# Optimization experiments

Measured on AMD Instinct MI355X. Metric: run time of the kernel, lower is better.

The kernel has to match this reference:

```python
import jax, jax.numpy as jnp
import numpy as np
import math

D_MODEL = 1024
N_HEADS = 16
DK = D_MODEL // N_HEADS


def setup_inputs() -> dict:
    key = jax.random.key(0)
    kx, kqkv, kproj = jax.random.split(key, 3)
    B, T = 4, 2048
    x = jax.random.normal(kx, (B, T, D_MODEL), dtype=jnp.float32)
    # torch Linear weight is [out, in]; y = x @ W.T
    W_qkv = jax.random.normal(kqkv, (3 * D_MODEL, D_MODEL), dtype=jnp.float32) * (1.0 / math.sqrt(D_MODEL))
    W_proj = jax.random.normal(kproj, (D_MODEL, D_MODEL), dtype=jnp.float32) * (1.0 / math.sqrt(D_MODEL))
    return {"x": x, "W_qkv": W_qkv, "W_proj": W_proj}


def reference(x, W_qkv, W_proj):
    B, T, D = x.shape
    qkv = jnp.einsum("btd,ed->bte", x, W_qkv)  # [B,T,3D]
    q, k, v = jnp.split(qkv, 3, axis=-1)
    # [B,T,D] -> [B,H,T,dk]
    def heads(t):
        return t.reshape(B, T, N_HEADS, DK).transpose(0, 2, 1, 3)
    q, k, v = heads(q), heads(k), heads(v)
    scale = 1.0 / math.sqrt(DK)
    att = jnp.einsum("bhqd,bhkd->bhqk", q, k) * scale  # [B,H,T,T]
    att = jax.nn.softmax(att, axis=-1)
    out = jnp.einsum("bhqk,bhkd->bhqd", att, v)  # [B,H,T,dk]
    out = out.transpose(0, 2, 1, 3).reshape(B, T, D)
    return jnp.einsum("btd,ed->bte", out, W_proj)
```

## Files before the change

kernel.cpp:

```cpp
#include <hip/hip_runtime.h>
#include <hip/hip_bf16.h>

#define D_MODEL 1024
#define N_HEADS 16
#define DK 64
#define B_SZ 4
#define T_SEQ 2048
#define M_ROWS (B_SZ * T_SEQ)
#define QK_SCALE_LOG2 0.18033688f

typedef short bf16x8 __attribute__((ext_vector_type(8)));
typedef float f32x4  __attribute__((ext_vector_type(4)));

__device__ inline unsigned short f32_to_bf16(float f) {
    union { float f; unsigned int u; } v; v.f = f;
    unsigned int r = v.u + 0x7fff + ((v.u >> 16) & 1);
    return (unsigned short)(r >> 16);
}
__device__ inline unsigned int pack_bf16x2(float a, float b) {
    __hip_bfloat162 t = __float22bfloat162_rn(make_float2(a, b));
    union { __hip_bfloat162 v; unsigned int u; } c; c.v = t;
    return c.u;
}

__global__ __launch_bounds__(256) void cast_bf16(
    const float* __restrict__ src, unsigned short* __restrict__ dst,
    int n, int nscaled, float s)
{
    for (int i = (blockIdx.x * 256 + threadIdx.x) * 4; i < n;
         i += gridDim.x * 256 * 4) {
        float4 v = *(const float4*)(src + i);
        const float sc = (i < nscaled) ? s : 1.0f;
        ushort4 h;
        h.x = f32_to_bf16(v.x * sc); h.y = f32_to_bf16(v.y * sc);
        h.z = f32_to_bf16(v.z * sc); h.w = f32_to_bf16(v.w * sc);
        *(ushort4*)(dst + i) = h;
    }
}

template <typename OutT>
__global__ __launch_bounds__(256) void gemm_bf16_nt(
    const unsigned short* __restrict__ A, const unsigned short* __restrict__ B,
    OutT* __restrict__ C, int M, int N, int K)
{
    __shared__ __align__(16) unsigned short sA[128 * 32];
    __shared__ __align__(16) unsigned short sB[128 * 32];

    const int t    = threadIdx.x;
    const int wave = t >> 6;
    const int lane = t & 63;
    const int l15  = lane & 15;
    const int quad = lane >> 4;
    const int m0   = blockIdx.y * 128;
    const int n0   = blockIdx.x * 128;

    const unsigned short* gplane = (wave < 2) ? A : B;
    unsigned short* lplane = (wave < 2) ? sA : sB;
    const int row0 = ((wave < 2) ? m0 : n0) + (wave & 1) * 64;
    const int lds0 = (wave & 1) * 2048;
    const unsigned short* gbase =
        gplane + (size_t)(row0 + (lane >> 2)) * K + (lane & 3) * 8;

    f32x4 acc[4][4];
#pragma unroll
    for (int i = 0; i < 4; ++i)
#pragma unroll
        for (int j = 0; j < 4; ++j) acc[i][j] = (f32x4){0.f, 0.f, 0.f, 0.f};

    const int wr = (wave >> 1) * 64;
    const int wc = (wave & 1) * 64;

    for (int k0 = 0; k0 < K; k0 += 32) {
#pragma unroll
        for (int i = 0; i < 4; ++i) {
            __builtin_amdgcn_global_load_lds(
                (const __attribute__((address_space(1))) unsigned int*)
                    (gbase + k0 + (size_t)i * 16 * K),
                (__attribute__((address_space(3))) unsigned int*)
                    (lplane + lds0 + i * 512),
                16, 0, 0);
        }
        __syncthreads();

        bf16x8 a[4], b[4];
#pragma unroll
        for (int f = 0; f < 4; ++f) {
            a[f] = *(const bf16x8*)&sA[(wr + f * 16 + l15) * 32 + quad * 8];
            b[f] = *(const bf16x8*)&sB[(wc + f * 16 + l15) * 32 + quad * 8];
        }
#pragma unroll
        for (int mi = 0; mi < 4; ++mi)
#pragma unroll
            for (int ni = 0; ni < 4; ++ni)
                acc[mi][ni] = __builtin_amdgcn_mfma_f32_16x16x32_bf16(
                    a[mi], b[ni], acc[mi][ni], 0, 0, 0);
        __syncthreads();
    }

#pragma unroll
    for (int mi = 0; mi < 4; ++mi)
#pragma unroll
        for (int r = 0; r < 4; ++r) {
            OutT* crow =
                C + (size_t)(m0 + wr + mi * 16 + quad * 4 + r) * N + n0 + wc + l15;
#pragma unroll
            for (int ni = 0; ni < 4; ++ni) {
                if constexpr (sizeof(OutT) == 2)
                    crow[ni * 16] = (OutT)f32_to_bf16(acc[mi][ni][r]);
                else
                    crow[ni * 16] = (OutT)acc[mi][ni][r];
            }
        }
}

__global__ __launch_bounds__(256) void prep_vt(
    const unsigned short* __restrict__ qkvb, unsigned short* __restrict__ vt)
{
    __shared__ unsigned short VT_s[64][132];
    const int t  = threadIdx.x;
    const int b  = blockIdx.z, h = blockIdx.y;
    const int t0 = blockIdx.x * 128;
    const unsigned short* vb = qkvb + (size_t)(b * T_SEQ) * (3 * D_MODEL)
                               + 2 * D_MODEL + h * DK;
#pragma unroll
    for (int it = 0; it < 8; ++it) {
        const int trow = (t >> 4) + it * 16;
        const int dk0  = (t & 15) * 4;
        ushort4 v = *(const ushort4*)(vb + (size_t)(t0 + trow) * (3 * D_MODEL) + dk0);
        VT_s[dk0 + 0][trow] = v.x; VT_s[dk0 + 1][trow] = v.y;
        VT_s[dk0 + 2][trow] = v.z; VT_s[dk0 + 3][trow] = v.w;
    }
    __syncthreads();

    const int c     = t >> 4;
    const int p8    = c * 8;
    const int sbase = (p8 & ~31) + ((p8 >> 3) & 3) * 4;
    unsigned short* dst =
        vt + (((size_t)((b * N_HEADS + h) * (T_SEQ / 128) + blockIdx.x) * 16 + c)
              * 64) * 8;
#pragma unroll
    for (int dd = 0; dd < 4; ++dd) {
        const int d = (t & 15) + dd * 16;
        ushort4 a  = *(const ushort4*)&VT_s[d][sbase];
        ushort4 b4 = *(const ushort4*)&VT_s[d][sbase + 16];
        union { ushort4 p[2]; uint4 v; } pk;
        pk.p[0] = a; pk.p[1] = b4;
        *(uint4*)(dst + d * 8) = pk.v;
    }
}

__global__ __launch_bounds__(256, 4) void attn_mfma(
    const unsigned short* __restrict__ qkvb,
    const unsigned short* __restrict__ vt,
    unsigned short* __restrict__ ob)
{
    __shared__ __align__(16) unsigned short Ksw[2][128 * 64];

    const int t    = threadIdx.x;
    const int wave = t >> 6;
    const int lane = t & 63;
    const int l15  = t & 15;
    const int quad = lane >> 4;
    const int swz  = l15 & 7;

    const int b  = blockIdx.z;
    const int h  = blockIdx.y;
    const int q0 = blockIdx.x * 128;

    bf16x8 qa[2][2];
#pragma unroll
    for (int qs = 0; qs < 2; ++qs) {
        const unsigned short* qrow =
            qkvb + ((size_t)(b * T_SEQ) + q0 + wave * 32 + qs * 16 + l15)
                   * (3 * D_MODEL) + h * DK;
        qa[qs][0] = *(const bf16x8*)(qrow + quad * 8);
        qa[qs][1] = *(const bf16x8*)(qrow + 32 + quad * 8);
    }

    f32x4 O[2][4], Lacc[2];
#pragma unroll
    for (int qs = 0; qs < 2; ++qs) {
        Lacc[qs] = (f32x4){0.f, 0.f, 0.f, 0.f};
#pragma unroll
        for (int nd = 0; nd < 4; ++nd) O[qs][nd] = (f32x4){0.f, 0.f, 0.f, 0.f};
    }

    const short one_bf = (short)0x3F80;
    const bf16x8 ones8 = {one_bf, one_bf, one_bf, one_bf,
                          one_bf, one_bf, one_bf, one_bf};

    const unsigned short* kbase =
        qkvb + (size_t)(b * T_SEQ) * (3 * D_MODEL) + D_MODEL + h * DK;
    const unsigned short* vbase =
        vt + (size_t)(b * N_HEADS + h) * DK * T_SEQ;

    const int krl  = wave * 32 + (lane >> 3);
    const int kcol = ((lane & 7) ^ (lane >> 3)) * 8;

#pragma unroll
    for (int i = 0; i < 4; ++i) {
        const int rk = krl + i * 8;
        __builtin_amdgcn_global_load_lds(
            (const __attribute__((address_space(1))) unsigned int*)
                (kbase + (size_t)rk * (3 * D_MODEL) + kcol),
            (__attribute__((address_space(3))) unsigned int*)
                (&Ksw[0][(wave * 4 + i) * 512]),
            16, 0, 0);
    }

    const int NT = T_SEQ / 128;
    for (int tile = 0; tile < NT; ++tile) {
        __syncthreads();

        if (tile + 1 < NT) {
            const int c0n = (tile + 1) * 128;
            const int nb  = (tile + 1) & 1;
#pragma unroll
            for (int i = 0; i < 4; ++i) {
                const int rk = krl + i * 8;
                __builtin_amdgcn_global_load_lds(
                    (const __attribute__((address_space(1))) unsigned int*)
                        (kbase + (size_t)(c0n + rk) * (3 * D_MODEL) + kcol),
                    (__attribute__((address_space(3))) unsigned int*)
                        (&Ksw[nb][(wave * 4 + i) * 512]),
                    16, 0, 0);
            }
        }

        const int cb = tile & 1;
        const unsigned short* vtile = vbase + (size_t)tile * (16 * 64 * 8);
        const unsigned short* vlane = vtile + quad * 512 + l15 * 8;
#pragma unroll
        for (int half = 0; half < 2; ++half) {
            f32x4 S[2][4];
#pragma unroll
            for (int qs = 0; qs < 2; ++qs)
#pragma unroll
                for (int nf = 0; nf < 4; ++nf) S[qs][nf] = (f32x4){0.f, 0.f, 0.f, 0.f};

            __builtin_amdgcn_s_setprio(1);
#pragma unroll
            for (int ks = 0; ks < 2; ++ks) {
                const int ch = ks * 4 + quad;
#pragma unroll
                for (int nf = 0; nf < 4; ++nf) {
                    const int row = half * 64 + nf * 16 + l15;
                    const bf16x8 kf =
                        *(const bf16x8*)&Ksw[cb][row * 64 + ((ch ^ swz) * 8)];
                    S[0][nf] = __builtin_amdgcn_mfma_f32_16x16x32_bf16(
                        kf, qa[0][ks], S[0][nf], 0, 0, 0);
                    S[1][nf] = __builtin_amdgcn_mfma_f32_16x16x32_bf16(
                        kf, qa[1][ks], S[1][nf], 0, 0, 0);
                }
            }
            __builtin_amdgcn_s_setprio(0);

#pragma unroll
            for (int gl = 0; gl < 2; ++gl) {
                bf16x8 pf[2];
#pragma unroll
                for (int qs = 0; qs < 2; ++qs) {
                    union { uint4 u; bf16x8 v; } cv;
                    const f32x4 s0 = S[qs][2 * gl];
                    const f32x4 s1 = S[qs][2 * gl + 1];
                    cv.u.x = pack_bf16x2(__builtin_amdgcn_exp2f(s0[0]),
                                         __builtin_amdgcn_exp2f(s0[1]));
                    cv.u.y = pack_bf16x2(__builtin_amdgcn_exp2f(s0[2]),
                                         __builtin_amdgcn_exp2f(s0[3]));
                    cv.u.z = pack_bf16x2(__builtin_amdgcn_exp2f(s1[0]),
                                         __builtin_amdgcn_exp2f(s1[1]));
                    cv.u.w = pack_bf16x2(__builtin_amdgcn_exp2f(s1[2]),
                                         __builtin_amdgcn_exp2f(s1[3]));
                    pf[qs] = cv.v;
                }
                const int g = half * 2 + gl;
                const unsigned short* vptr = vlane + (size_t)g * 2048;
                __builtin_amdgcn_s_setprio(1);
#pragma unroll
                for (int nd = 0; nd < 4; ++nd) {
                    const bf16x8 vb = *(const bf16x8*)(vptr + nd * 128);
                    O[0][nd] = __builtin_amdgcn_mfma_f32_16x16x32_bf16(
                        pf[0], vb, O[0][nd], 0, 0, 0);
                    O[1][nd] = __builtin_amdgcn_mfma_f32_16x16x32_bf16(
                        pf[1], vb, O[1][nd], 0, 0, 0);
                }
                Lacc[0] = __builtin_amdgcn_mfma_f32_16x16x32_bf16(
                    pf[0], ones8, Lacc[0], 0, 0, 0);
                Lacc[1] = __builtin_amdgcn_mfma_f32_16x16x32_bf16(
                    pf[1], ones8, Lacc[1], 0, 0, 0);
                __builtin_amdgcn_s_setprio(0);
            }
        }
    }

#pragma unroll
    for (int qs = 0; qs < 2; ++qs)
#pragma unroll
        for (int r = 0; r < 4; ++r) {
            const float invl = 1.0f / Lacc[qs][r];
            const size_t rowbase =
                ((size_t)(b * T_SEQ) + q0 + wave * 32 + qs * 16 + quad * 4 + r)
                * D_MODEL + h * DK + l15;
#pragma unroll
            for (int nd = 0; nd < 4; ++nd)
                ob[rowbase + nd * 16] = f32_to_bf16(O[qs][nd][r] * invl);
        }
}

extern "C" void kernel_launch(void* const* d_in, const int* in_sizes, int n_in,
                              void* d_out, int out_size, void* d_ws, size_t ws_size,
                              hipStream_t stream)
{
    const float* x      = (const float*)d_in[0];
    const float* W_qkv  = (const float*)d_in[1];
    const float* W_proj = (const float*)d_in[2];
    float* out = (float*)d_out;

    const size_t XN = (size_t)M_ROWS * D_MODEL;
    const size_t WQ = (size_t)3 * D_MODEL * D_MODEL;
    const size_t WP = (size_t)D_MODEL * D_MODEL;
    unsigned short* xb   = (unsigned short*)d_ws;
    unsigned short* wqb  = xb + XN;
    unsigned short* wpb  = wqb + WQ;
    unsigned short* qkvb = wpb + WP;
    unsigned short* vtb  = qkvb + (size_t)M_ROWS * 3 * D_MODEL;
    unsigned short* ab   = xb;

    dim3 blk(256);
    cast_bf16<<<512, blk, 0, stream>>>(x, xb, (int)XN, 0, 1.0f);
    cast_bf16<<<256, blk, 0, stream>>>(W_qkv, wqb, (int)WQ,
                                       D_MODEL * D_MODEL, QK_SCALE_LOG2);
    cast_bf16<<<128, blk, 0, stream>>>(W_proj, wpb, (int)WP, 0, 1.0f);

    gemm_bf16_nt<unsigned short>
        <<<dim3(3 * D_MODEL / 128, M_ROWS / 128), blk, 0, stream>>>(
        xb, wqb, qkvb, M_ROWS, 3 * D_MODEL, D_MODEL);

    prep_vt<<<dim3(T_SEQ / 128, N_HEADS, B_SZ), blk, 0, stream>>>(qkvb, vtb);
    attn_mfma<<<dim3(T_SEQ / 128, N_HEADS, B_SZ), blk, 0, stream>>>(
        qkvb, vtb, ab);

    gemm_bf16_nt<float>
        <<<dim3(D_MODEL / 128, M_ROWS / 128), blk, 0, stream>>>(
        ab, wpb, out, M_ROWS, D_MODEL, D_MODEL);
}
```

Measured before the change: 291.3 us.

## Double GEMM K-tile to 64 with XOR-swizzled LDS and XCD-aware block remap

Doubles the K step of the bf16 GEMM tile to 64, which halves the number of barrier pairs per output tile. LDS rows are XOR-swizzled so the wider rows do not cause bank conflicts on the fragment reads. The 2D grid is flattened and block IDs are remapped so that neighbouring tiles land on the same XCD, aiming for better L2 reuse. In exchange, LDS use per block doubles and launch bounds ask for 4 blocks per CU, which adds register pressure.

```diff
diff --git a/kernel.cpp b/kernel.cpp
--- a/kernel.cpp
+++ b/kernel.cpp
@@ -39,27 +39,33 @@
 }
 
 template <typename OutT>
-__global__ __launch_bounds__(256) void gemm_bf16_nt(
+__global__ __launch_bounds__(256, 4) void gemm_bf16_nt(
     const unsigned short* __restrict__ A, const unsigned short* __restrict__ B,
-    OutT* __restrict__ C, int M, int N, int K)
-{
-    __shared__ __align__(16) unsigned short sA[128 * 32];
-    __shared__ __align__(16) unsigned short sB[128 * 32];
+    OutT* __restrict__ C, int M, int N, int K, int nbx)
+{
+    __shared__ __align__(16) unsigned short sA[128 * 64];
+    __shared__ __align__(16) unsigned short sB[128 * 64];
 
     const int t    = threadIdx.x;
     const int wave = t >> 6;
     const int lane = t & 63;
     const int l15  = lane & 15;
     const int quad = lane >> 4;
-    const int m0   = blockIdx.y * 128;
-    const int n0   = blockIdx.x * 128;
+    const int swz  = l15 & 7;
+
+    const int cpx = gridDim.x >> 3;
+    const int wg  = (blockIdx.x & 7) * cpx + (blockIdx.x >> 3);
+    const int n0  = (wg % nbx) * 128;
+    const int m0  = (wg / nbx) * 128;
 
     const unsigned short* gplane = (wave < 2) ? A : B;
     unsigned short* lplane = (wave < 2) ? sA : sB;
     const int row0 = ((wave < 2) ? m0 : n0) + (wave & 1) * 64;
-    const int lds0 = (wave & 1) * 2048;
+    unsigned short* lbase = lplane + (wave & 1) * 4096;
+    const int rsub = lane >> 3;
+    const int cg   = (lane & 7) ^ rsub;
     const unsigned short* gbase =
-        gplane + (size_t)(row0 + (lane >> 2)) * K + (lane & 3) * 8;
+        gplane + (size_t)(row0 + rsub) * K + cg * 8;
 
     f32x4 acc[4][4];
 #pragma unroll
@@ -70,30 +76,35 @@
     const int wr = (wave >> 1) * 64;
     const int wc = (wave & 1) * 64;
 
-    for (int k0 = 0; k0 < K; k0 += 32) {
-#pragma unroll
-        for (int i = 0; i < 4; ++i) {
+    for (int k0 = 0; k0 < K; k0 += 64) {
+#pragma unroll
+        for (int i = 0; i < 8; ++i) {
             __builtin_amdgcn_global_load_lds(
                 (const __attribute__((address_space(1))) unsigned int*)
-                    (gbase + k0 + (size_t)i * 16 * K),
+                    (gbase + k0 + (size_t)(i * 8) * K),
                 (__attribute__((address_space(3))) unsigned int*)
-                    (lplane + lds0 + i * 512),
+                    (lbase + i * 512),
                 16, 0, 0);
         }
         __syncthreads();
 
-        bf16x8 a[4], b[4];
-#pragma unroll
-        for (int f = 0; f < 4; ++f) {
-            a[f] = *(const bf16x8*)&sA[(wr + f * 16 + l15) * 32 + quad * 8];
-            b[f] = *(const bf16x8*)&sB[(wc + f * 16 + l15) * 32 + quad * 8];
-        }
-#pragma unroll
-        for (int mi = 0; mi < 4; ++mi)
-#pragma unroll
-            for (int ni = 0; ni < 4; ++ni)
-                acc[mi][ni] = __builtin_amdgcn_mfma_f32_16x16x32_bf16(
-                    a[mi], b[ni], acc[mi][ni], 0, 0, 0);
+#pragma unroll
+        for (int kk = 0; kk < 2; ++kk) {
+            bf16x8 a[4], b[4];
+            const int ch = kk * 4 + quad;
+            const int co = (ch ^ swz) * 8;
+#pragma unroll
+            for (int f = 0; f < 4; ++f) {
+                a[f] = *(const bf16x8*)&sA[(wr + f * 16 + l15) * 64 + co];
+                b[f] = *(const bf16x8*)&sB[(wc + f * 16 + l15) * 64 + co];
+            }
+#pragma unroll
+            for (int mi = 0; mi < 4; ++mi)
+#pragma unroll
+                for (int ni = 0; ni < 4; ++ni)
+                    acc[mi][ni] = __builtin_amdgcn_mfma_f32_16x16x32_bf16(
+                        a[mi], b[ni], acc[mi][ni], 0, 0, 0);
+        }
         __syncthreads();
     }
 
@@ -333,14 +344,14 @@
     cast_bf16<<<128, blk, 0, stream>>>(W_proj, wpb, (int)WP, 0, 1.0f);
 
     gemm_bf16_nt<unsigned short>
-        <<<dim3(3 * D_MODEL / 128, M_ROWS / 128), blk, 0, stream>>>(
-        xb, wqb, qkvb, M_ROWS, 3 * D_MODEL, D_MODEL);
+        <<<dim3((3 * D_MODEL / 128) * (M_ROWS / 128)), blk, 0, stream>>>(
+        xb, wqb, qkvb, M_ROWS, 3 * D_MODEL, D_MODEL, 3 * D_MODEL / 128);
 
     prep_vt<<<dim3(T_SEQ / 128, N_HEADS, B_SZ), blk, 0, stream>>>(qkvb, vtb);
     attn_mfma<<<dim3(T_SEQ / 128, N_HEADS, B_SZ), blk, 0, stream>>>(
         qkvb, vtb, ab);
 
     gemm_bf16_nt<float>
-        <<<dim3(D_MODEL / 128, M_ROWS / 128), blk, 0, stream>>>(
-        ab, wpb, out, M_ROWS, D_MODEL, D_MODEL);
-}
+        <<<dim3((D_MODEL / 128) * (M_ROWS / 128)), blk, 0, stream>>>(
+        ab, wpb, out, M_ROWS, D_MODEL, D_MODEL, D_MODEL / 128);
+}
```

New measurement: 275.6 us. 5.4% less time.
